# Performance work log

Measured on AMD Instinct MI355X. Metric: run time of the kernel, lower is better.

Reference implementation:

```python
import jax, jax.numpy as jnp
import numpy as np

B, T, IN, H, L = 512, 75, 96, 1024, 3
HARDTANH_LIMIT = 1.0


def setup_inputs() -> dict:
    key = jax.random.key(0)
    ks = jax.random.split(key, 32)
    inp = {
        'inputs': jax.random.normal(ks[0], (B, T, IN), jnp.float32),
        'hiddens': jax.random.normal(ks[1], (L, B, H), jnp.float32),
        'cells': jax.random.normal(ks[2], (L, B, H), jnp.float32),
    }
    s = 1.0 / np.sqrt(H)
    kidx = 3
    for i in range(L):
        in_dim = IN if i == 0 else H
        inp[f'Wih{i}'] = jax.random.uniform(ks[kidx], (4 * H, in_dim), jnp.float32, -s, s); kidx += 1
        inp[f'Whh{i}'] = jax.random.uniform(ks[kidx], (4 * H, H), jnp.float32, -s, s); kidx += 1
        inp[f'bih{i}'] = jax.random.uniform(ks[kidx], (4 * H,), jnp.float32, -s, s); kidx += 1
        inp[f'bhh{i}'] = jax.random.uniform(ks[kidx], (4 * H,), jnp.float32, -s, s); kidx += 1
    inp['fc_w'] = jax.random.uniform(ks[kidx], (IN, H), jnp.float32, -s, s); kidx += 1
    inp['fc_b'] = jax.random.uniform(ks[kidx], (IN,), jnp.float32, -s, s)
    return inp


def _lstm_cell(x, h, c, Wih, Whh, bih, bhh):
    # PyTorch LSTMCell gate order: i, f, g, o
    gates = x @ Wih.T + bih + h @ Whh.T + bhh  # [B, 4H]
    i, f, g, o = jnp.split(gates, 4, axis=-1)
    c_new = jax.nn.sigmoid(f) * c + jax.nn.sigmoid(i) * jnp.tanh(g)
    h_new = jax.nn.sigmoid(o) * jnp.tanh(c_new)
    return h_new, c_new


def reference(inputs, hiddens, cells,
              Wih0, Whh0, bih0, bhh0,
              Wih1, Whh1, bih1, bhh1,
              Wih2, Whh2, bih2, bhh2,
              fc_w, fc_b):
    params = [(Wih0, Whh0, bih0, bhh0),
              (Wih1, Whh1, bih1, bhh1),
              (Wih2, Whh2, bih2, bhh2)]
    # dropout p=0.0 -> identity
    out0 = inputs[..., 0, :]  # [B, IN]

    def step(carry, _):
        hs, cs, out = carry
        x = jax.lax.stop_gradient(out)  # .detach() in the original
        new_h, new_c = [], []
        for i, (Wih, Whh, bih, bhh) in enumerate(params):
            xi = x if i == 0 else new_h[i - 1]
            h, c = _lstm_cell(xi, hs[i], cs[i], Wih, Whh, bih, bhh)
            new_h.append(h)
            new_c.append(c)
        out = new_h[-1] @ fc_w.T + fc_b
        out = jnp.clip(out, -HARDTANH_LIMIT, HARDTANH_LIMIT)  # Hardtanh
        return (jnp.stack(new_h), jnp.stack(new_c), out), out

    (_, _, _), outs = jax.lax.scan(step, (hiddens, cells, out0), None, length=inputs.shape[-2])
    return jnp.swapaxes(outs, 0, 1)  # [B, T, IN]
```

## Files before the change

### kernel.cpp

```cpp
#include <hip/hip_runtime.h>
#include <cstdint>
#include <cstddef>


typedef unsigned short u16;
typedef float v4f __attribute__((ext_vector_type(4)));
typedef short v8s __attribute__((ext_vector_type(8)));
typedef u16   v8u16 __attribute__((ext_vector_type(8)));

#define BATCH 512
#define H_DIM 1024
#define GATES 4096
#define T_STEPS 75
#define IN_DIM 96
#define K0P 1152
#define K12 2048
#define NBLK 256

__device__ __forceinline__ float bf2f(u16 u) {
    unsigned int x = ((unsigned int)u) << 16;
    return __builtin_bit_cast(float, x);
}
__device__ __forceinline__ u16 f2bf(float f) {
    unsigned int x = __builtin_bit_cast(unsigned int, f);
    x += 0x7fffu + ((x >> 16) & 1u);
    return (u16)(x >> 16);
}
__device__ __forceinline__ void gload16(const void* g, void* l) {
    __builtin_amdgcn_global_load_lds(
        (const __attribute__((address_space(1))) void*)g,
        (__attribute__((address_space(3))) void*)l, 16, 0, 0);
}
__device__ __forceinline__ void st_agent_u32(unsigned int* p, unsigned int v) {
    __hip_atomic_store(p, v, __ATOMIC_RELAXED, __HIP_MEMORY_SCOPE_AGENT);
}
__device__ __forceinline__ unsigned int ld_agent_u32(const unsigned int* p) {
    return __hip_atomic_load(p, __ATOMIC_RELAXED, __HIP_MEMORY_SCOPE_AGENT);
}

__device__ __forceinline__ void grid_sync(int* bar, int g, bool acq) {
    __syncthreads();
    if (threadIdx.x == 0) {
        int old = __hip_atomic_fetch_add(&bar[(blockIdx.x & 7) * 32], 1,
                                         __ATOMIC_RELAXED, __HIP_MEMORY_SCOPE_AGENT);
        if (old + 1 == 32 * g) {
            int r = __hip_atomic_fetch_add(&bar[256], 1,
                                           __ATOMIC_RELAXED, __HIP_MEMORY_SCOPE_AGENT);
            if (r + 1 == 8 * g)
                __hip_atomic_store(&bar[288], g,
                                   __ATOMIC_RELAXED, __HIP_MEMORY_SCOPE_AGENT);
        }
        int spins = 0;
        while (__hip_atomic_load(&bar[288],
                                 __ATOMIC_RELAXED, __HIP_MEMORY_SCOPE_AGENT) < g) {
            if (++spins > (1 << 17)) break;
            __builtin_amdgcn_s_sleep(1);
        }
        if (acq)
            __builtin_amdgcn_fence(__ATOMIC_ACQUIRE, "agent");
    }
    __syncthreads();
}

__device__ __forceinline__ void gemm_stage(
    char* smem, const u16* __restrict__ A, const u16* __restrict__ W,
    int K, int nk, v4f bv, v4f& cc,
    u16* __restrict__ h1, int h1s, u16* __restrict__ h2, int h2s,
    int bm, int j0)
{
    u16* sA = (u16*)smem;
    u16* sB = (u16*)(smem + 32768);

    const int tid  = threadIdx.x;
    const int lane = tid & 63;
    const int wid  = tid >> 6;
    const int wm   = (wid >> 1) * 16;
    const int wn   = (wid & 1) * 64;
    const int l15  = lane & 15;
    const int lq   = lane >> 4;

    v4f acc[4];
    #pragma unroll
    for (int nf = 0; nf < 4; ++nf) {
        v4f tv = {bv[nf], bv[nf], bv[nf], bv[nf]};
        acc[nf] = tv;
    }

    const int srow = tid >> 3;
    const int kcs  = ((tid & 7) ^ (srow & 7)) << 3;

    auto stage = [&](int b, int k0) {
        u16* sa = sA + b * 4096;
        u16* sb = sB + b * 8192;
        gload16(A + (size_t)(bm + srow) * K + k0 + kcs, sa + tid * 8);
        #pragma unroll
        for (int q = 0; q < 2; ++q) {
            const int fr = q * 64 + srow;
            gload16(W + (size_t)((fr >> 5) * H_DIM + j0 + (fr & 31)) * K + k0 + kcs,
                    sb + q * 4096 + tid * 8);
        }
    };

    {
        const int npre = nk < 3 ? nk : 3;
        for (int p = 0; p < npre; ++p) stage(p, p * 64);
    }

    #pragma unroll 1
    for (int tt = 0; tt < nk; ++tt) {
        const int cur = tt & 3;
        if (tt + 3 < nk) stage((tt + 3) & 3, (tt + 3) * 64);
        const int ahead = (nk - 1 - tt) < 3 ? (nk - 1 - tt) : 3;
        if (ahead == 3)      asm volatile("s_waitcnt vmcnt(9)" ::: "memory");
        else if (ahead == 2) asm volatile("s_waitcnt vmcnt(6)" ::: "memory");
        else if (ahead == 1) asm volatile("s_waitcnt vmcnt(3)" ::: "memory");
        else                 asm volatile("s_waitcnt vmcnt(0)" ::: "memory");
        asm volatile("s_barrier" ::: "memory");

        const char* sa = (const char*)(sA + cur * 4096);
        const char* sb = (const char*)(sB + cur * 8192);
        v8s af[2], bfr[4][2];
        #pragma unroll
        for (int ks = 0; ks < 2; ++ks) {
            const int row = wm + l15;
            const int ch  = ks * 4 + lq;
            af[ks] = *(const v8s*)(sa + row * 128 + (((ch ^ (row & 7))) << 4));
        }
        #pragma unroll
        for (int nf = 0; nf < 4; ++nf)
            #pragma unroll
            for (int ks = 0; ks < 2; ++ks) {
                const int row = wn + nf * 16 + l15;
                const int ch  = ks * 4 + lq;
                bfr[nf][ks] = *(const v8s*)(sb + row * 128 + (((ch ^ (row & 7))) << 4));
            }
        #pragma unroll
        for (int ks = 0; ks < 2; ++ks)
            #pragma unroll
            for (int nf = 0; nf < 4; ++nf)
                acc[nf] = __builtin_amdgcn_mfma_f32_16x16x32_bf16(
                    af[ks], bfr[nf][ks], acc[nf], 0, 0, 0);
        asm volatile("s_barrier" ::: "memory");
    }

    float* sG = (float*)smem;
    #pragma unroll
    for (int nf = 0; nf < 4; ++nf)
        #pragma unroll
        for (int r = 0; r < 4; ++r)
            sG[(wm + lq * 4 + r) * 132 + wn + nf * 16 + l15] = acc[nf][r];
    __syncthreads();

    const int erow = tid >> 3;
    const int jj   = (tid & 7) * 4;
    const int gb   = bm + erow;
    const float* sGr = sG + erow * 132;
    v4f n0;
    u16 hv[4];
    #pragma unroll
    for (int q = 0; q < 4; ++q) {
        const float gi = sGr[      jj + q];
        const float gf = sGr[32  + jj + q];
        const float gg = sGr[64  + jj + q];
        const float go = sGr[96  + jj + q];
        const float cv = cc[q];
        const float ii = 1.f / (1.f + __expf(-gi));
        const float ff = 1.f / (1.f + __expf(-gf));
        const float g2 = tanhf(gg);
        const float oo = 1.f / (1.f + __expf(-go));
        const float cq = ff * cv + ii * g2;
        n0[q] = cq;
        hv[q] = f2bf(oo * tanhf(cq));
    }
    cc = n0;
    unsigned int* d1 = (unsigned int*)(h1 + (size_t)gb * h1s + j0 + jj);
    #pragma unroll
    for (int w2 = 0; w2 < 2; ++w2) {
        unsigned int val = (unsigned int)hv[2 * w2] | ((unsigned int)hv[2 * w2 + 1] << 16);
        st_agent_u32(d1 + w2, val);
    }
    if (h2) {
        unsigned int* d2 = (unsigned int*)(h2 + (size_t)gb * h2s + j0 + jj);
        #pragma unroll
        for (int w2 = 0; w2 < 2; ++w2) {
            unsigned int val = (unsigned int)hv[2 * w2] | ((unsigned int)hv[2 * w2 + 1] << 16);
            st_agent_u32(d2 + w2, val);
        }
    }
}

__device__ __forceinline__ void fc_stage(
    char* smem, const u16* __restrict__ h2, int h2s,
    const u16* __restrict__ w, const float* __restrict__ fcb,
    float* __restrict__ out, u16* __restrict__ xdst, int t, int id)
{
    float* sh = (float*)smem;
    const int tid  = threadIdx.x;
    const int half = tid >> 8;
    const int htid = tid & 255;
    const int b    = id * 2 + half;
    const unsigned int* hp = (const unsigned int*)(h2 + (size_t)b * h2s + htid * 4);
    #pragma unroll
    for (int w4 = 0; w4 < 2; ++w4) {
        unsigned int u = ld_agent_u32(hp + w4);
        sh[half * H_DIM + htid * 4 + 2 * w4]     = bf2f((u16)(u & 0xffffu));
        sh[half * H_DIM + htid * 4 + 2 * w4 + 1] = bf2f((u16)(u >> 16));
    }
    __syncthreads();
    if (htid < IN_DIM) {
        const u16* wr = w + (size_t)htid * H_DIM;
        const float* shr = sh + half * H_DIM;
        float acc = fcb[htid];
        #pragma unroll 4
        for (int k = 0; k < H_DIM; k += 8) {
            v8u16 wv = *(const v8u16*)(wr + k);
            #pragma unroll
            for (int q = 0; q < 8; ++q) acc += shr[k + q] * bf2f(wv[q]);
        }
        acc = fminf(1.f, fmaxf(-1.f, acc));
        out[(size_t)b * (T_STEPS * IN_DIM) + t * IN_DIM + htid] = acc;
        float o2 = __shfl_xor(acc, 1);
        if ((htid & 1) == 0) {
            unsigned int val = (unsigned int)f2bf(acc) | ((unsigned int)f2bf(o2) << 16);
            st_agent_u32((unsigned int*)(xdst + (size_t)b * K0P + htid), val);
        }
    }
}

__global__ __launch_bounds__(512, 1) void lstm_all_k(
    const u16* __restrict__ w0, const u16* __restrict__ w1, const u16* __restrict__ w2,
    u16* A00, u16* A01, u16* A10, u16* A11, u16* A20, u16* A21,
    const u16* __restrict__ fcw, const float* __restrict__ bsum,
    const float* __restrict__ cells, const float* __restrict__ fcb,
    float* __restrict__ out, int* bar)
{
    __shared__ __align__(16) char smem[98304];

    const int tid  = threadIdx.x;
    const int lane = tid & 63;
    const int wid  = tid >> 6;
    const int wn   = (wid & 1) * 64;
    const int l15  = lane & 15;

    const int id    = blockIdx.x;
    const int panel = (id & 7) * 4 + (id >> 6);
    const int mblk  = (id >> 3) & 7;
    const int bm    = mblk * 64;
    const int j0    = panel * 32;

    v4f bv0, bv1, bv2;
    #pragma unroll
    for (int nf = 0; nf < 4; ++nf) {
        const int ncol = wn + nf * 16 + l15;
        const int idx  = (ncol >> 5) * H_DIM + j0 + (ncol & 31);
        bv0[nf] = bsum[idx];
        bv1[nf] = bsum[GATES + idx];
        bv2[nf] = bsum[2 * GATES + idx];
    }

    const int erow = tid >> 3;
    const int jj   = (tid & 7) * 4;
    const int gb   = bm + erow;
    v4f c0, c1, c2;
    {
        const float* cr = cells + (size_t)gb * H_DIM + j0 + jj;
        c0 = *(const v4f*)cr;
        cr += (size_t)BATCH * H_DIM;
        c1 = *(const v4f*)cr;
        cr += (size_t)BATCH * H_DIM;
        c2 = *(const v4f*)cr;
    }

    int g = 0;
    #pragma unroll 1
    for (int t = 0; t < T_STEPS; ++t) {
        const int pr = t & 1;
        u16* A0r = pr ? A01 : A00;  u16* A0w = pr ? A00 : A01;
        u16* A1r = pr ? A11 : A10;  u16* A1w = pr ? A10 : A11;
        u16* A2r = pr ? A21 : A20;  u16* A2w = pr ? A20 : A21;

        gemm_stage(smem, A0r, w0, K0P, K0P / 64, bv0, c0,
                   A0w + IN_DIM, K0P, A1r, K12, bm, j0);
        grid_sync(bar, ++g, false);
        gemm_stage(smem, A1r, w1, K12, K12 / 64, bv1, c1,
                   A1w + H_DIM, K12, A2r, K12, bm, j0);
        grid_sync(bar, ++g, false);
        gemm_stage(smem, A2r, w2, K12, K12 / 64, bv2, c2,
                   A2w + H_DIM, K12, (u16*)nullptr, 0, bm, j0);
        grid_sync(bar, ++g, false);
        fc_stage(smem, A2w + H_DIM, K12, fcw, fcb, out, A0w, t, id);
        grid_sync(bar, ++g, true);
    }
}

__global__ __launch_bounds__(256) void convpack_k(
    const float* __restrict__ src, int srcStride,
    u16* __restrict__ dst, int dstStride, int cols8, long total8)
{
    long i = (long)blockIdx.x * 256 + threadIdx.x;
    if (i >= total8) return;
    const int r  = (int)(i / cols8);
    const int cc = (int)(i - (long)r * cols8) * 8;
    const float* s = src + (size_t)r * srcStride + cc;
    v4f a = *(const v4f*)s;
    v4f b = *(const v4f*)(s + 4);
    v8u16 o;
    #pragma unroll
    for (int q = 0; q < 4; ++q) { o[q] = f2bf(a[q]); o[4 + q] = f2bf(b[q]); }
    *(v8u16*)(dst + (size_t)r * dstStride + cc) = o;
}

__global__ __launch_bounds__(256) void zero16_k(
    u16* __restrict__ dst, int dstStride, int cols8, long total8)
{
    long i = (long)blockIdx.x * 256 + threadIdx.x;
    if (i >= total8) return;
    const int r  = (int)(i / cols8);
    const int cc = (int)(i - (long)r * cols8) * 8;
    v8u16 z = {0, 0, 0, 0, 0, 0, 0, 0};
    *(v8u16*)(dst + (size_t)r * dstStride + cc) = z;
}

__global__ __launch_bounds__(256) void add_k(
    const float* __restrict__ a, const float* __restrict__ b,
    float* __restrict__ o, int n)
{
    int i = blockIdx.x * 256 + threadIdx.x;
    if (i < n) o[i] = a[i] + b[i];
}

extern "C" void kernel_launch(void* const* d_in, const int* in_sizes, int n_in,
                              void* d_out, int out_size, void* d_ws, size_t ws_size,
                              hipStream_t stream)
{
    const float* inputs  = (const float*)d_in[0];
    const float* hiddens = (const float*)d_in[1];
    const float* cells   = (const float*)d_in[2];
    const float* Wih[3]  = {(const float*)d_in[3], (const float*)d_in[7],  (const float*)d_in[11]};
    const float* Whh[3]  = {(const float*)d_in[4], (const float*)d_in[8],  (const float*)d_in[12]};
    const float* bih[3]  = {(const float*)d_in[5], (const float*)d_in[9],  (const float*)d_in[13]};
    const float* bhh[3]  = {(const float*)d_in[6], (const float*)d_in[10], (const float*)d_in[14]};
    const float* fc_w    = (const float*)d_in[15];
    const float* fc_b    = (const float*)d_in[16];
    float* out = (float*)d_out;

    char* p = (char*)d_ws;
    auto take = [&](size_t bytes) -> void* {
        void* r = p; p += (bytes + 255) & ~(size_t)255; return r;
    };
    const int Kl[3]  = {K0P, K12, K12};
    const int Kin[3] = {IN_DIM, H_DIM, H_DIM};
    u16* wcat[3];
    for (int l = 0; l < 3; ++l) wcat[l] = (u16*)take((size_t)GATES * Kl[l] * 2);
    u16* Ab[3][2];
    for (int l = 0; l < 3; ++l)
        for (int q = 0; q < 2; ++q) Ab[l][q] = (u16*)take((size_t)BATCH * Kl[l] * 2);
    u16*   fcwb = (u16*)take((size_t)IN_DIM * H_DIM * 2);
    float* bsum = (float*)take((size_t)3 * GATES * 4);
    int*   bar  = (int*)take(8192);
    if ((size_t)(p - (char*)d_ws) > ws_size) return;

    auto pack = [&](const float* s, int ss, u16* d, int ds, int rows, int cols) {
        long t8 = (long)rows * (cols / 8);
        convpack_k<<<(int)((t8 + 255) / 256), 256, 0, stream>>>(s, ss, d, ds, cols / 8, t8);
    };
    auto zero = [&](u16* d, int ds, int rows, int cols) {
        long t8 = (long)rows * (cols / 8);
        zero16_k<<<(int)((t8 + 255) / 256), 256, 0, stream>>>(d, ds, cols / 8, t8);
    };

    for (int l = 0; l < 3; ++l) {
        pack(Wih[l], Kin[l], wcat[l],           Kl[l], GATES, Kin[l]);
        pack(Whh[l], H_DIM,  wcat[l] + Kin[l],  Kl[l], GATES, H_DIM);
    }
    zero(wcat[0] + IN_DIM + H_DIM, K0P, GATES, K0P - IN_DIM - H_DIM);
    pack(fc_w, H_DIM, fcwb, H_DIM, IN_DIM, H_DIM);

    for (int l = 0; l < 3; ++l)
        pack(hiddens + (size_t)l * BATCH * H_DIM, H_DIM,
             Ab[l][0] + Kin[l], Kl[l], BATCH, H_DIM);
    pack(inputs, T_STEPS * IN_DIM, Ab[0][0], K0P, BATCH, IN_DIM);
    zero(Ab[0][0] + IN_DIM + H_DIM, K0P, BATCH, K0P - IN_DIM - H_DIM);
    zero(Ab[0][1] + IN_DIM + H_DIM, K0P, BATCH, K0P - IN_DIM - H_DIM);

    for (int l = 0; l < 3; ++l)
        add_k<<<16, 256, 0, stream>>>(bih[l], bhh[l], bsum + l * GATES, GATES);
    hipMemsetAsync(bar, 0, 8192, stream);

    lstm_all_k<<<NBLK, 512, 0, stream>>>(
        wcat[0], wcat[1], wcat[2],
        Ab[0][0], Ab[0][1], Ab[1][0], Ab[1][1], Ab[2][0], Ab[2][1],
        fcwb, bsum, cells, fc_b, out,
        bar);
}
```

Before: 4.517 ms.

## Prepack weights in MFMA fragment order and load directly into registers

Weights are repacked on the host side into the per-lane fragment order the MFMA B operand expects, so each wave loads its weight fragments straight from global memory into registers with coalesced 16-byte loads. This removes the shared-memory staging and LDS reads of the weight tile, halves LDS use, and double-buffers weight fragments in registers across K steps. The cost is more register pressure, a shorter A-tile prefetch depth (2 instead of 3), and weight reuse no longer shared through LDS.

```diff
diff --git a/kernel.cpp b/kernel.cpp
--- a/kernel.cpp
+++ b/kernel.cpp
@@ -66,10 +66,9 @@
     char* smem, const u16* __restrict__ A, const u16* __restrict__ W,
     int K, int nk, v4f bv, v4f& cc,
     u16* __restrict__ h1, int h1s, u16* __restrict__ h2, int h2s,
-    int bm, int j0)
+    int bm, int j0, int panel)
 {
     u16* sA = (u16*)smem;
-    u16* sB = (u16*)(smem + 32768);
 
     const int tid  = threadIdx.x;
     const int lane = tid & 63;
@@ -78,6 +77,7 @@
     const int wn   = (wid & 1) * 64;
     const int l15  = lane & 15;
     const int lq   = lane >> 4;
+    (void)wn;
 
     v4f acc[4];
     #pragma unroll
@@ -88,59 +88,61 @@
 
     const int srow = tid >> 3;
     const int kcs  = ((tid & 7) ^ (srow & 7)) << 3;
-
-    auto stage = [&](int b, int k0) {
-        u16* sa = sA + b * 4096;
-        u16* sb = sB + b * 8192;
-        gload16(A + (size_t)(bm + srow) * K + k0 + kcs, sa + tid * 8);
-        #pragma unroll
-        for (int q = 0; q < 2; ++q) {
-            const int fr = q * 64 + srow;
-            gload16(W + (size_t)((fr >> 5) * H_DIM + j0 + (fr & 31)) * K + k0 + kcs,
-                    sb + q * 4096 + tid * 8);
-        }
-    };
-
-    {
-        const int npre = nk < 3 ? nk : 3;
-        for (int p = 0; p < npre; ++p) stage(p, p * 64);
-    }
-
-    #pragma unroll 1
-    for (int tt = 0; tt < nk; ++tt) {
-        const int cur = tt & 3;
-        if (tt + 3 < nk) stage((tt + 3) & 3, (tt + 3) * 64);
-        const int ahead = (nk - 1 - tt) < 3 ? (nk - 1 - tt) : 3;
-        if (ahead == 3)      asm volatile("s_waitcnt vmcnt(9)" ::: "memory");
-        else if (ahead == 2) asm volatile("s_waitcnt vmcnt(6)" ::: "memory");
-        else if (ahead == 1) asm volatile("s_waitcnt vmcnt(3)" ::: "memory");
-        else                 asm volatile("s_waitcnt vmcnt(0)" ::: "memory");
+    const size_t abase = (size_t)(bm + srow) * K + kcs;
+    auto stageA = [&](int b, int t) {
+        gload16(A + abase + t * 64, sA + b * 4096 + tid * 8);
+    };
+
+    const int kper = K >> 5;
+    const u16* wb[4];
+    #pragma unroll
+    for (int nf = 0; nf < 4; ++nf)
+        wb[nf] = W + (((size_t)((panel * 2 + (wid & 1)) * 4 + nf) * kper) << 9)
+                   + lane * 8;
+    v8s wA[4][2], wB[4][2];
+    auto loadW = [&](int t, v8s (&w)[4][2]) {
+        #pragma unroll
+        for (int nf = 0; nf < 4; ++nf)
+            #pragma unroll
+            for (int s = 0; s < 2; ++s)
+                w[nf][s] = *(const v8s*)(wb[nf] + ((size_t)(2 * t + s) << 9));
+    };
+
+    stageA(0, 0);
+    if (nk > 1) stageA(1, 1);
+    loadW(0, wA);
+    if (nk > 1) loadW(1, wB);
+
+    auto ITER = [&](int t, v8s (&w)[4][2]) {
+        if (t + 2 < nk) stageA((t + 2) & 3, t + 2);
+        const int rem = nk - 1 - t;
+        if (rem >= 2)      asm volatile("s_waitcnt vmcnt(18)" ::: "memory");
+        else if (rem == 1) asm volatile("s_waitcnt vmcnt(9)"  ::: "memory");
+        else               asm volatile("s_waitcnt vmcnt(0)"  ::: "memory");
         asm volatile("s_barrier" ::: "memory");
 
-        const char* sa = (const char*)(sA + cur * 4096);
-        const char* sb = (const char*)(sB + cur * 8192);
-        v8s af[2], bfr[4][2];
+        const char* sa = (const char*)(sA + (t & 3) * 4096);
+        v8s af[2];
         #pragma unroll
         for (int ks = 0; ks < 2; ++ks) {
             const int row = wm + l15;
             const int ch  = ks * 4 + lq;
-            af[ks] = *(const v8s*)(sa + row * 128 + (((ch ^ (row & 7))) << 4));
-        }
-        #pragma unroll
-        for (int nf = 0; nf < 4; ++nf)
-            #pragma unroll
-            for (int ks = 0; ks < 2; ++ks) {
-                const int row = wn + nf * 16 + l15;
-                const int ch  = ks * 4 + lq;
-                bfr[nf][ks] = *(const v8s*)(sb + row * 128 + (((ch ^ (row & 7))) << 4));
-            }
+            af[ks] = *(const v8s*)(sa + row * 128 + ((ch ^ (row & 7)) << 4));
+        }
         #pragma unroll
         for (int ks = 0; ks < 2; ++ks)
             #pragma unroll
             for (int nf = 0; nf < 4; ++nf)
                 acc[nf] = __builtin_amdgcn_mfma_f32_16x16x32_bf16(
-                    af[ks], bfr[nf][ks], acc[nf], 0, 0, 0);
+                    af[ks], w[nf][ks], acc[nf], 0, 0, 0);
+        if (t + 2 < nk) loadW(t + 2, w);
         asm volatile("s_barrier" ::: "memory");
+    };
+
+    #pragma unroll 1
+    for (int t2 = 0; t2 < nk; t2 += 2) {
+        ITER(t2, wA);
+        ITER(t2 + 1, wB);
     }
 
     float* sG = (float*)smem;
@@ -148,7 +150,7 @@
     for (int nf = 0; nf < 4; ++nf)
         #pragma unroll
         for (int r = 0; r < 4; ++r)
-            sG[(wm + lq * 4 + r) * 132 + wn + nf * 16 + l15] = acc[nf][r];
+            sG[(wm + lq * 4 + r) * 132 + (wid & 1) * 64 + nf * 16 + l15] = acc[nf][r];
     __syncthreads();
 
     const int erow = tid >> 3;
@@ -234,7 +236,7 @@
     const float* __restrict__ cells, const float* __restrict__ fcb,
     float* __restrict__ out, int* bar)
 {
-    __shared__ __align__(16) char smem[98304];
+    __shared__ __align__(16) char smem[49152];
 
     const int tid  = threadIdx.x;
     const int lane = tid & 63;
@@ -280,13 +282,13 @@
         u16* A2r = pr ? A21 : A20;  u16* A2w = pr ? A20 : A21;
 
         gemm_stage(smem, A0r, w0, K0P, K0P / 64, bv0, c0,
-                   A0w + IN_DIM, K0P, A1r, K12, bm, j0);
+                   A0w + IN_DIM, K0P, A1r, K12, bm, j0, panel);
         grid_sync(bar, ++g, false);
         gemm_stage(smem, A1r, w1, K12, K12 / 64, bv1, c1,
-                   A1w + H_DIM, K12, A2r, K12, bm, j0);
+                   A1w + H_DIM, K12, A2r, K12, bm, j0, panel);
         grid_sync(bar, ++g, false);
         gemm_stage(smem, A2r, w2, K12, K12 / 64, bv2, c2,
-                   A2w + H_DIM, K12, (u16*)nullptr, 0, bm, j0);
+                   A2w + H_DIM, K12, (u16*)nullptr, 0, bm, j0, panel);
         grid_sync(bar, ++g, false);
         fc_stage(smem, A2w + H_DIM, K12, fcw, fcb, out, A0w, t, id);
         grid_sync(bar, ++g, true);
@@ -308,6 +310,36 @@
     #pragma unroll
     for (int q = 0; q < 4; ++q) { o[q] = f2bf(a[q]); o[4 + q] = f2bf(b[q]); }
     *(v8u16*)(dst + (size_t)r * dstStride + cc) = o;
+}
+
+__global__ __launch_bounds__(256) void packw_k(
+    const float* __restrict__ Wih, const float* __restrict__ Whh,
+    int Kin, int K, u16* __restrict__ dst, long nchunks)
+{
+    long i = (long)blockIdx.x * 256 + threadIdx.x;
+    if (i >= nchunks) return;
+    const int kper = K >> 5;
+    const int l    = (int)(i & 63);
+    const int ks   = (int)((i >> 6) % kper);
+    const int r2   = (int)((i >> 6) / kper);
+    const int nf   = r2 & 3, wnh = (r2 >> 2) & 1, panel = r2 >> 3;
+    const int rip  = wnh * 64 + nf * 16 + (l & 15);
+    const int grow = (rip >> 5) * 1024 + panel * 32 + (rip & 31);
+    const int k    = ks * 32 + (l >> 4) * 8;
+    v8u16 o;
+    if (k < Kin) {
+        const float* s = Wih + (size_t)grow * Kin + k;
+        #pragma unroll
+        for (int q = 0; q < 8; ++q) o[q] = f2bf(s[q]);
+    } else if (k < Kin + 1024) {
+        const float* s = Whh + (size_t)grow * 1024 + (k - Kin);
+        #pragma unroll
+        for (int q = 0; q < 8; ++q) o[q] = f2bf(s[q]);
+    } else {
+        #pragma unroll
+        for (int q = 0; q < 8; ++q) o[q] = 0;
+    }
+    *(v8u16*)(dst + i * 8) = o;
 }
 
 __global__ __launch_bounds__(256) void zero16_k(
@@ -350,8 +382,8 @@
     };
     const int Kl[3]  = {K0P, K12, K12};
     const int Kin[3] = {IN_DIM, H_DIM, H_DIM};
-    u16* wcat[3];
-    for (int l = 0; l < 3; ++l) wcat[l] = (u16*)take((size_t)GATES * Kl[l] * 2);
+    u16* wfr[3];
+    for (int l = 0; l < 3; ++l) wfr[l] = (u16*)take((size_t)GATES * Kl[l] * 2);
     u16* Ab[3][2];
     for (int l = 0; l < 3; ++l)
         for (int q = 0; q < 2; ++q) Ab[l][q] = (u16*)take((size_t)BATCH * Kl[l] * 2);
@@ -370,10 +402,10 @@
     };
 
     for (int l = 0; l < 3; ++l) {
-        pack(Wih[l], Kin[l], wcat[l],           Kl[l], GATES, Kin[l]);
-        pack(Whh[l], H_DIM,  wcat[l] + Kin[l],  Kl[l], GATES, H_DIM);
-    }
-    zero(wcat[0] + IN_DIM + H_DIM, K0P, GATES, K0P - IN_DIM - H_DIM);
+        long nch = (long)512 * Kl[l];
+        packw_k<<<(int)((nch + 255) / 256), 256, 0, stream>>>(
+            Wih[l], Whh[l], Kin[l], Kl[l], wfr[l], nch);
+    }
     pack(fc_w, H_DIM, fcwb, H_DIM, IN_DIM, H_DIM);
 
     for (int l = 0; l < 3; ++l)
@@ -388,7 +420,7 @@
     hipMemsetAsync(bar, 0, 8192, stream);
 
     lstm_all_k<<<NBLK, 512, 0, stream>>>(
-        wcat[0], wcat[1], wcat[2],
+        wfr[0], wfr[1], wfr[2],
         Ab[0][0], Ab[0][1], Ab[1][0], Ab[1][1], Ab[2][0], Ab[2][1],
         fcwb, bsum, cells, fc_b, out,
         bar);
```

Measured after the change: 6.326 ms. 40.0% more time.
